# Kernel tuning notes

Measured on AMD Instinct MI355X. Metric: run time of the kernel, lower is better.

Reference implementation:

```python
import jax, jax.numpy as jnp
import numpy as np

N_NODES = 100000
HIDDEN = 64
N_LAYERS = 4
N_EDGES = 800000
EPS = 1e-5  # equinox RMSNorm default


def rmsnorm(x, w):
    # per-node RMSNorm over last dim, learned scale, no bias
    inv = jax.lax.rsqrt(jnp.mean(x * x, axis=-1, keepdims=True) + EPS)
    return x * inv * w


def setup_inputs() -> dict:
    key = jax.random.key(0)
    ks = jax.random.split(key, 5)
    x = jax.random.normal(ks[0], (N_NODES, HIDDEN), dtype=jnp.float32)
    # eqx Linear weight (out,in), init ~ U(-1/sqrt(in), 1/sqrt(in)); randn*scale is fine for a baseline
    scale = 1.0 / np.sqrt(HIDDEN)
    conv_w = jax.random.normal(ks[1], (N_LAYERS, HIDDEN, HIDDEN), dtype=jnp.float32) * scale
    hid_w = jax.random.normal(ks[2], (N_LAYERS, HIDDEN, HIDDEN), dtype=jnp.float32) * scale
    conv_norm_w = jnp.ones((N_LAYERS, HIDDEN), dtype=jnp.float32)
    hid_norm_w = jnp.ones((N_LAYERS, HIDDEN), dtype=jnp.float32)
    row = jax.random.randint(ks[3], (N_EDGES,), 0, N_NODES, dtype=jnp.int32)
    col = jax.random.randint(ks[4], (N_EDGES,), 0, N_NODES, dtype=jnp.int32)
    return {"x": x, "conv_w": conv_w, "conv_norm_w": conv_norm_w,
            "hid_w": hid_w, "hid_norm_w": hid_norm_w, "row": row, "col": col}


def reference(x, conv_w, conv_norm_w, hid_w, hid_norm_w, row, col):
    n_nodes = x.shape[0]

    def step(h, params):
        cw, cnw, hw, hnw = params
        # GConvLayer: linear (no bias) -> relu -> sparse adjacency aggregation -> residual RMSNorm
        m = jax.nn.relu(h @ cw.T)                                  # [n_nodes, d]
        agg = jax.ops.segment_sum(m[col], row, num_segments=n_nodes)  # a @ m (unweighted COO)
        h = rmsnorm(h + agg, cnw)
        # HiddenLayer: linear -> relu -> residual RMSNorm
        y = jax.nn.relu(h @ hw.T)
        h = rmsnorm(h + y, hnw)
        return h, None

    x, _ = jax.lax.scan(step, x, (conv_w, conv_norm_w, hid_w, hid_norm_w))
    return x
```

## Files before the change

### kernel.cpp

```cpp
#include <hip/hip_runtime.h>
#include <hip/hip_bf16.h>

#define HIDDEN 64
#define EPS 1e-5f
#define NPB 64
#define WST 72

typedef __attribute__((ext_vector_type(8))) short bf16x8;
typedef __attribute__((ext_vector_type(4))) float f32x4;

__device__ __forceinline__ unsigned short f2b(float x) {
    __hip_bfloat16 b = __float2bfloat16(x);
    return *(unsigned short*)&b;
}
__device__ __forceinline__ float b2f(unsigned short u) {
    unsigned int ui = (unsigned int)u << 16;
    return *(float*)&ui;
}
__device__ __forceinline__ float b2f_lo(unsigned int u) { unsigned int ui = u << 16; return *(float*)&ui; }
__device__ __forceinline__ float b2f_hi(unsigned int u) { unsigned int ui = u & 0xffff0000u; return *(float*)&ui; }


__global__ __launch_bounds__(256) void hist_rank_kernel(const int* __restrict__ row,
                                                        int* __restrict__ cnt,
                                                        int* __restrict__ erank, int e) {
    int stride = gridDim.x * blockDim.x;
    for (int i = blockIdx.x * blockDim.x + threadIdx.x; i < e; i += stride) {
        int r = row[i];
        erank[i] = atomicAdd(&cnt[r], 1);
    }
}

__global__ __launch_bounds__(256) void block_sum_kernel(const int* __restrict__ cnt,
                                                        int* __restrict__ bsum, int n) {
    __shared__ int wsum[4];
    int tid = threadIdx.x;
    int i = blockIdx.x * 256 + tid;
    int v = (i < n) ? cnt[i] : 0;
#pragma unroll
    for (int off = 32; off > 0; off >>= 1) v += __shfl_xor(v, off, 64);
    if ((tid & 63) == 0) wsum[tid >> 6] = v;
    __syncthreads();
    if (tid == 0) bsum[blockIdx.x] = wsum[0] + wsum[1] + wsum[2] + wsum[3];
}

__global__ __launch_bounds__(256) void scan_final_kernel(const int* __restrict__ cnt,
                                                         const int* __restrict__ bsum,
                                                         int* __restrict__ row_ptr,
                                                         int n, int nb) {
    __shared__ int wred[4];
    __shared__ int wsum[4];
    __shared__ int wexcl[4];
    __shared__ int s_prev;
    __shared__ int s_tot;
    int b = blockIdx.x;
    int tid = threadIdx.x;
    int lane = tid & 63;
    int w = tid >> 6;
    int acc = 0;
    for (int j = tid; j < b; j += 256) acc += bsum[j];
#pragma unroll
    for (int off = 32; off > 0; off >>= 1) acc += __shfl_xor(acc, off, 64);
    if (lane == 0) wred[w] = acc;
    int i = b * 256 + tid;
    int v = (i < n) ? cnt[i] : 0;
    int sc = v;
#pragma unroll
    for (int off = 1; off < 64; off <<= 1) {
        int t = __shfl_up(sc, off, 64);
        if (lane >= off) sc += t;
    }
    if (lane == 63) wsum[w] = sc;
    __syncthreads();
    if (tid == 0) {
        s_prev = wred[0] + wred[1] + wred[2] + wred[3];
        int a = 0;
#pragma unroll
        for (int j = 0; j < 4; j++) { wexcl[j] = a; a += wsum[j]; }
        s_tot = a;
    }
    __syncthreads();
    if (i < n) row_ptr[i] = s_prev + wexcl[w] + (sc - v);
    if (b == nb - 1 && tid == 0) row_ptr[n] = s_prev + s_tot;
}

__global__ __launch_bounds__(256) void fill_kernel(const int* __restrict__ row,
                                                   const int* __restrict__ col,
                                                   const int* __restrict__ row_ptr,
                                                   const int* __restrict__ erank,
                                                   int* __restrict__ ecol, int e, int n) {
    int cls = blockIdx.x & 7;
    int sub = blockIdx.x >> 3;
    int nsub = gridDim.x >> 3;
    int lo = (int)(((long long)n * cls) >> 3);
    int hi = (int)(((long long)n * (cls + 1)) >> 3);
    for (int i = sub * 256 + threadIdx.x; i < e; i += nsub * 256) {
        int r = row[i];
        if (r >= lo && r < hi) {
            int pos = row_ptr[r] + erank[i];
            ecol[pos] = col[i];
        }
    }
}

__global__ __launch_bounds__(256) void wconv_kernel(const float* __restrict__ cw,
                                                    const float* __restrict__ hw,
                                                    unsigned short* __restrict__ wbt, int L) {
    int idx = blockIdx.x * blockDim.x + threadIdx.x;
    int total = 2 * L * 4096;
    if (idx >= total) return;
    int mat = idx >> 12;
    int rem = idx & 4095;
    const float* src = (mat < L) ? (cw + (size_t)mat * 4096) : (hw + (size_t)(mat - L) * 4096);
    wbt[idx] = f2b(src[rem]);
}


__device__ __forceinline__ void mfma_tile(const unsigned short* s_a,
                                          const unsigned short* s_b,
                                          int l16, int quad, int wbase, f32x4 acc[4]) {
    const unsigned short* ap = &s_a[(size_t)(wbase + l16) * WST + quad * 8];
    const unsigned short* bp = &s_b[(size_t)l16 * WST + quad * 8];
#pragma unroll
    for (int kt = 0; kt < 2; kt++) {
        bf16x8 a = *(const bf16x8*)(ap + kt * 32);
#pragma unroll
        for (int nt = 0; nt < 4; nt++) {
            bf16x8 b = *(const bf16x8*)(bp + (size_t)nt * 16 * WST + kt * 32);
            acc[nt] = __builtin_amdgcn_mfma_f32_16x16x32_bf16(a, b, acc[nt], 0, 0, 0);
        }
    }
}

__device__ __forceinline__ void stage_wb(const unsigned short* __restrict__ wsrc,
                                         unsigned short* s_wb, int tid) {
    for (int i = tid; i < 512; i += 256) {
        int r = i >> 3, seg = i & 7;
        *(uint4*)(&s_wb[r * WST + seg * 8]) = ((const uint4*)(wsrc + r * 64))[seg];
    }
}


__global__ __launch_bounds__(256) void mm_relu_kernel(const float* __restrict__ h,
                                                      const unsigned short* __restrict__ wb,
                                                      __hip_bfloat16* __restrict__ m, int n) {
    __shared__ unsigned short s_hb[NPB * WST];
    __shared__ unsigned short s_wb[64 * WST];
    int tid = threadIdx.x;
    int base = blockIdx.x * NPB;
    stage_wb(wb, s_wb, tid);
    for (int i = tid; i < 512; i += 256) {
        int r = i >> 3, seg = i & 7;
        if (base + r < n) {
            const float4* hp = (const float4*)(h + (size_t)(base + r) * HIDDEN + seg * 8);
            float4 ha = hp[0], hb = hp[1];
            uint4 p;
            p.x = (unsigned int)f2b(ha.x) | ((unsigned int)f2b(ha.y) << 16);
            p.y = (unsigned int)f2b(ha.z) | ((unsigned int)f2b(ha.w) << 16);
            p.z = (unsigned int)f2b(hb.x) | ((unsigned int)f2b(hb.y) << 16);
            p.w = (unsigned int)f2b(hb.z) | ((unsigned int)f2b(hb.w) << 16);
            *(uint4*)(&s_hb[r * WST + seg * 8]) = p;
        } else {
            *(uint4*)(&s_hb[r * WST + seg * 8]) = make_uint4(0u, 0u, 0u, 0u);
        }
    }
    __syncthreads();
    int lane = tid & 63, wave = tid >> 6;
    int quad = lane >> 4, l16 = lane & 15;
    int wbase = wave * 16;
    f32x4 acc[4];
    acc[0] = (f32x4){0.f,0.f,0.f,0.f}; acc[1] = (f32x4){0.f,0.f,0.f,0.f};
    acc[2] = (f32x4){0.f,0.f,0.f,0.f}; acc[3] = (f32x4){0.f,0.f,0.f,0.f};
    mfma_tile(s_hb, s_wb, l16, quad, wbase, acc);
    unsigned short* mo = (unsigned short*)m;
#pragma unroll
    for (int r = 0; r < 4; r++) {
        int node = base + wbase + quad * 4 + r;
        if (node < n) {
#pragma unroll
            for (int nt = 0; nt < 4; nt++)
                mo[(size_t)node * HIDDEN + nt * 16 + l16] = f2b(fmaxf(acc[nt][r], 0.f));
        }
    }
}


__global__ __launch_bounds__(256) void fused_layer_kernel(
        const float* hf, const __hip_bfloat16* hb_in,
        const __hip_bfloat16* __restrict__ m_in,
        const unsigned short* __restrict__ hwb,
        const unsigned short* cwb_next,
        const int* __restrict__ row_ptr, const int* __restrict__ ecol,
        const float* __restrict__ cnw, const float* __restrict__ hnw,
        float* out_f32, __hip_bfloat16* hb_new, __hip_bfloat16* m_out, int n) {
    __shared__ unsigned short s_hb[NPB * WST];
    __shared__ unsigned short s_wb[64 * WST];
    __shared__ unsigned short s_wb2[64 * WST];
    int tid = threadIdx.x;
    int base = blockIdx.x * NPB;
    int lane = tid & 63, wave = tid >> 6;

    stage_wb(hwb, s_wb, tid);
    if (cwb_next) stage_wb(cwb_next, s_wb2, tid);

    int grp = lane >> 3;
    int sl = lane & 7;
    int sbase = grp * 8;
    const float4* cp = (const float4*)(cnw + 8 * sl);
    float4 c0 = cp[0], c1 = cp[1];
    const unsigned short* mi = (const unsigned short*)m_in;

#pragma unroll
    for (int rnd = 0; rnd < 2; rnd++) {
        int nl = wave * 16 + rnd * 8 + grp;
        int node = base + nl;
        uint4 pb = make_uint4(0u, 0u, 0u, 0u);
        if (node < n) {
            float s[8];
            if (hf) {
                const float4* hp = (const float4*)(hf + (size_t)node * HIDDEN + 8 * sl);
                float4 v0 = hp[0], v1 = hp[1];
                s[0] = v0.x; s[1] = v0.y; s[2] = v0.z; s[3] = v0.w;
                s[4] = v1.x; s[5] = v1.y; s[6] = v1.z; s[7] = v1.w;
            } else {
                uint4 u = *(const uint4*)((const unsigned short*)hb_in + (size_t)node * HIDDEN + 8 * sl);
                s[0] = b2f_lo(u.x); s[1] = b2f_hi(u.x);
                s[2] = b2f_lo(u.y); s[3] = b2f_hi(u.y);
                s[4] = b2f_lo(u.z); s[5] = b2f_hi(u.z);
                s[6] = b2f_lo(u.w); s[7] = b2f_hi(u.w);
            }
            int beg = row_ptr[node];
            int end = row_ptr[node + 1];
            float p0[8], p1[8];
#pragma unroll
            for (int q = 0; q < 8; q++) { p0[q] = 0.f; p1[q] = 0.f; }
            for (int b0 = beg; b0 < end; b0 += 8) {
                int idx = b0 + sl;
                int myc = ecol[idx < end ? idx : end - 1];
                int cnt = end - b0;
                if (cnt > 8) cnt = 8;
                int c[8];
#pragma unroll
                for (int j = 0; j < 8; j++) c[j] = __shfl(myc, sbase + j, 64);
                uint4 u[8];
#pragma unroll
                for (int j = 0; j < 8; j++)
                    u[j] = *(const uint4*)(mi + (size_t)c[j] * HIDDEN + 8 * sl);
#pragma unroll
                for (int j = 0; j < 8; j++) {
                    bool ok = j < cnt;
                    float* p = (j & 1) ? p1 : p0;
                    p[0] += ok ? b2f_lo(u[j].x) : 0.f;
                    p[1] += ok ? b2f_hi(u[j].x) : 0.f;
                    p[2] += ok ? b2f_lo(u[j].y) : 0.f;
                    p[3] += ok ? b2f_hi(u[j].y) : 0.f;
                    p[4] += ok ? b2f_lo(u[j].z) : 0.f;
                    p[5] += ok ? b2f_hi(u[j].z) : 0.f;
                    p[6] += ok ? b2f_lo(u[j].w) : 0.f;
                    p[7] += ok ? b2f_hi(u[j].w) : 0.f;
                }
            }
            float ss = 0.f;
#pragma unroll
            for (int q = 0; q < 8; q++) {
                s[q] += p0[q] + p1[q];
                ss += s[q] * s[q];
            }
#pragma unroll
            for (int off = 4; off > 0; off >>= 1) ss += __shfl_xor(ss, off, 64);
            float inv = rsqrtf(ss * (1.0f / 64.0f) + EPS);
            pb.x = (unsigned int)f2b(s[0] * inv * c0.x) | ((unsigned int)f2b(s[1] * inv * c0.y) << 16);
            pb.y = (unsigned int)f2b(s[2] * inv * c0.z) | ((unsigned int)f2b(s[3] * inv * c0.w) << 16);
            pb.z = (unsigned int)f2b(s[4] * inv * c1.x) | ((unsigned int)f2b(s[5] * inv * c1.y) << 16);
            pb.w = (unsigned int)f2b(s[6] * inv * c1.z) | ((unsigned int)f2b(s[7] * inv * c1.w) << 16);
        }
        *(uint4*)(&s_hb[(size_t)nl * WST + 8 * sl]) = pb;
    }
    __syncthreads();

    int quad = lane >> 4, l16 = lane & 15;
    int wbase = wave * 16;
    f32x4 acc[4];
    acc[0] = (f32x4){0.f,0.f,0.f,0.f}; acc[1] = (f32x4){0.f,0.f,0.f,0.f};
    acc[2] = (f32x4){0.f,0.f,0.f,0.f}; acc[3] = (f32x4){0.f,0.f,0.f,0.f};
    mfma_tile(s_hb, s_wb, l16, quad, wbase, acc);

    float hv[4][4];
    float ssq[4] = {0.f, 0.f, 0.f, 0.f};
#pragma unroll
    for (int r = 0; r < 4; r++) {
        int nl = wbase + quad * 4 + r;
#pragma unroll
        for (int nt = 0; nt < 4; nt++) {
            float hres = b2f(s_hb[(size_t)nl * WST + nt * 16 + l16]);
            float v = hres + fmaxf(acc[nt][r], 0.f);
            hv[r][nt] = v;
            ssq[r] += v * v;
        }
    }
#pragma unroll
    for (int mk = 1; mk <= 8; mk <<= 1) {
#pragma unroll
        for (int r = 0; r < 4; r++) ssq[r] += __shfl_xor(ssq[r], mk, 64);
    }
    float nwv[4];
#pragma unroll
    for (int nt = 0; nt < 4; nt++) nwv[nt] = hnw[nt * 16 + l16];
#pragma unroll
    for (int r = 0; r < 4; r++) {
        float inv = rsqrtf(ssq[r] * (1.0f / 64.0f) + EPS);
#pragma unroll
        for (int nt = 0; nt < 4; nt++) hv[r][nt] *= inv * nwv[nt];
    }
    if (out_f32) {
#pragma unroll
        for (int r = 0; r < 4; r++) {
            int node = base + wbase + quad * 4 + r;
            if (node < n) {
#pragma unroll
                for (int nt = 0; nt < 4; nt++)
                    out_f32[(size_t)node * HIDDEN + nt * 16 + l16] = hv[r][nt];
            }
        }
    }
    if (hb_new) {
        unsigned short* ho = (unsigned short*)hb_new;
#pragma unroll
        for (int r = 0; r < 4; r++) {
            int node = base + wbase + quad * 4 + r;
            if (node < n) {
#pragma unroll
                for (int nt = 0; nt < 4; nt++)
                    ho[(size_t)node * HIDDEN + nt * 16 + l16] = f2b(hv[r][nt]);
            }
        }
    }

    if (!m_out) return;

#pragma unroll
    for (int r = 0; r < 4; r++) {
        int nl = wbase + quad * 4 + r;
#pragma unroll
        for (int nt = 0; nt < 4; nt++)
            s_hb[(size_t)nl * WST + nt * 16 + l16] = f2b(hv[r][nt]);
    }

    f32x4 acc2[4];
    acc2[0] = (f32x4){0.f,0.f,0.f,0.f}; acc2[1] = (f32x4){0.f,0.f,0.f,0.f};
    acc2[2] = (f32x4){0.f,0.f,0.f,0.f}; acc2[3] = (f32x4){0.f,0.f,0.f,0.f};
    mfma_tile(s_hb, s_wb2, l16, quad, wbase, acc2);
    unsigned short* mo = (unsigned short*)m_out;
#pragma unroll
    for (int r = 0; r < 4; r++) {
        int node = base + wbase + quad * 4 + r;
        if (node < n) {
#pragma unroll
            for (int nt = 0; nt < 4; nt++)
                mo[(size_t)node * HIDDEN + nt * 16 + l16] = f2b(fmaxf(acc2[nt][r], 0.f));
        }
    }
}


static inline size_t align_up(size_t x, size_t a) { return (x + a - 1) & ~(a - 1); }

extern "C" void kernel_launch(void* const* d_in, const int* in_sizes, int n_in,
                              void* d_out, int out_size, void* d_ws, size_t ws_size,
                              hipStream_t stream) {
    const float* x       = (const float*)d_in[0];
    const float* conv_w  = (const float*)d_in[1];
    const float* conv_nw = (const float*)d_in[2];
    const float* hid_w   = (const float*)d_in[3];
    const float* hid_nw  = (const float*)d_in[4];
    const int*   row     = (const int*)d_in[5];
    const int*   col     = (const int*)d_in[6];
    float* out = (float*)d_out;

    const int n = in_sizes[0] / HIDDEN;
    const int e = in_sizes[5];
    const int L = in_sizes[1] / 4096;

    size_t off = 0;
    char* ws = (char*)d_ws;
    __hip_bfloat16* mA = (__hip_bfloat16*)(ws + off);  off = align_up(off + (size_t)n * HIDDEN * 2, 16);
    __hip_bfloat16* mB = (__hip_bfloat16*)(ws + off);  off = align_up(off + (size_t)n * HIDDEN * 2, 16);
    __hip_bfloat16* hb1 = (__hip_bfloat16*)(ws + off); off = align_up(off + (size_t)n * HIDDEN * 2, 16);
    __hip_bfloat16* hb2 = (__hip_bfloat16*)(ws + off); off = align_up(off + (size_t)n * HIDDEN * 2, 16);
    unsigned short* wbt = (unsigned short*)(ws + off); off = align_up(off + (size_t)2 * L * 4096 * 2, 16);
    int* row_ptr = (int*)(ws + off);           off = align_up(off + (size_t)(n + 1) * 4, 16);
    int* cnt = (int*)(ws + off);               off = align_up(off + (size_t)n * 4, 16);
    int* bsum = (int*)(ws + off);              off = align_up(off + (size_t)1024 * 4, 16);
    int* erank = (int*)(ws + off);             off = align_up(off + (size_t)e * 4, 16);
    int* ecol = (int*)(ws + off);              off = align_up(off + (size_t)e * 4, 16);

    const int nb = (n + 255) / 256;

    hipMemsetAsync(cnt, 0, (size_t)n * 4, stream);
    hist_rank_kernel<<<1024, 256, 0, stream>>>(row, cnt, erank, e);
    block_sum_kernel<<<nb, 256, 0, stream>>>(cnt, bsum, n);
    scan_final_kernel<<<nb, 256, 0, stream>>>(cnt, bsum, row_ptr, n, nb);
    fill_kernel<<<1024, 256, 0, stream>>>(row, col, row_ptr, erank, ecol, e, n);

    wconv_kernel<<<(2 * L * 4096 + 255) / 256, 256, 0, stream>>>(conv_w, hid_w, wbt, L);

    const int blocks = (n + NPB - 1) / NPB;

    mm_relu_kernel<<<blocks, 256, 0, stream>>>(x, wbt, mA, n);

    const __hip_bfloat16* mi = mA;
    __hip_bfloat16* mo = mB;
    __hip_bfloat16* hin = nullptr;
    __hip_bfloat16* hout = hb1;
    for (int l = 0; l < L; l++) {
        bool last = (l == L - 1);
        fused_layer_kernel<<<blocks, 256, 0, stream>>>(
            (l == 0) ? x : nullptr, hin, mi,
            wbt + (size_t)(L + l) * 4096,
            last ? nullptr : (wbt + (size_t)(l + 1) * 4096),
            row_ptr, ecol,
            conv_nw + (size_t)l * HIDDEN, hid_nw + (size_t)l * HIDDEN,
            last ? out : nullptr,
            last ? nullptr : hout,
            last ? nullptr : mo, n);
        __hip_bfloat16* tmp = (__hip_bfloat16*)mi; mi = mo; mo = tmp;
        hin = hout;
        hout = (hout == hb1) ? hb2 : hb1;
    }
}
```

Before: 275.1 us.

## Use 4 lanes per node in gather with prefetched edge indices; load next-layer weights to registers

The gather/aggregation phase now assigns 4 lanes per node, each handling 16 features with two 16-byte loads per neighbor. This replaces the old 8 lanes per node over two rounds. The next batch of edge column indices is prefetched to overlap index loads with the gathers. The second shared-memory weight buffer is removed: the next layer's conv weights are loaded from global memory straight into MFMA B-fragment registers. This cuts LDS usage, which may raise occupancy, at the cost of more registers per thread and fewer loads in flight per batch of edges.

```diff
diff --git a/kernel.cpp b/kernel.cpp
--- a/kernel.cpp
+++ b/kernel.cpp
@@ -19,6 +19,9 @@
 }
 __device__ __forceinline__ float b2f_lo(unsigned int u) { unsigned int ui = u << 16; return *(float*)&ui; }
 __device__ __forceinline__ float b2f_hi(unsigned int u) { unsigned int ui = u & 0xffff0000u; return *(float*)&ui; }
+__device__ __forceinline__ unsigned int pk2(float a, float b) {
+    return (unsigned int)f2b(a) | ((unsigned int)f2b(b) << 16);
+}
 
 
 __global__ __launch_bounds__(256) void hist_rank_kernel(const int* __restrict__ row,
@@ -140,6 +143,17 @@
     }
 }
 
+__device__ __forceinline__ void acc8(float* p, uint4 u, bool ok) {
+    p[0] += ok ? b2f_lo(u.x) : 0.f;
+    p[1] += ok ? b2f_hi(u.x) : 0.f;
+    p[2] += ok ? b2f_lo(u.y) : 0.f;
+    p[3] += ok ? b2f_hi(u.y) : 0.f;
+    p[4] += ok ? b2f_lo(u.z) : 0.f;
+    p[5] += ok ? b2f_hi(u.z) : 0.f;
+    p[6] += ok ? b2f_lo(u.w) : 0.f;
+    p[7] += ok ? b2f_hi(u.w) : 0.f;
+}
+
 
 __global__ __launch_bounds__(256) void mm_relu_kernel(const float* __restrict__ h,
                                                       const unsigned short* __restrict__ wb,
@@ -155,10 +169,10 @@
             const float4* hp = (const float4*)(h + (size_t)(base + r) * HIDDEN + seg * 8);
             float4 ha = hp[0], hb = hp[1];
             uint4 p;
-            p.x = (unsigned int)f2b(ha.x) | ((unsigned int)f2b(ha.y) << 16);
-            p.y = (unsigned int)f2b(ha.z) | ((unsigned int)f2b(ha.w) << 16);
-            p.z = (unsigned int)f2b(hb.x) | ((unsigned int)f2b(hb.y) << 16);
-            p.w = (unsigned int)f2b(hb.z) | ((unsigned int)f2b(hb.w) << 16);
+            p.x = pk2(ha.x, ha.y);
+            p.y = pk2(ha.z, ha.w);
+            p.z = pk2(hb.x, hb.y);
+            p.w = pk2(hb.z, hb.w);
             *(uint4*)(&s_hb[r * WST + seg * 8]) = p;
         } else {
             *(uint4*)(&s_hb[r * WST + seg * 8]) = make_uint4(0u, 0u, 0u, 0u);
@@ -195,87 +209,96 @@
         float* out_f32, __hip_bfloat16* hb_new, __hip_bfloat16* m_out, int n) {
     __shared__ unsigned short s_hb[NPB * WST];
     __shared__ unsigned short s_wb[64 * WST];
-    __shared__ unsigned short s_wb2[64 * WST];
     int tid = threadIdx.x;
     int base = blockIdx.x * NPB;
     int lane = tid & 63, wave = tid >> 6;
 
     stage_wb(hwb, s_wb, tid);
-    if (cwb_next) stage_wb(cwb_next, s_wb2, tid);
-
-    int grp = lane >> 3;
-    int sl = lane & 7;
-    int sbase = grp * 8;
-    const float4* cp = (const float4*)(cnw + 8 * sl);
-    float4 c0 = cp[0], c1 = cp[1];
+
+    int g = lane >> 2;
+    int sl = lane & 3;
+    int gb = lane & ~3;
+    int nl = wave * 16 + g;
+    int node = base + nl;
+
+    const float4* cp = (const float4*)(cnw + 16 * sl);
+    float4 c0 = cp[0], c1 = cp[1], c2 = cp[2], c3 = cp[3];
     const unsigned short* mi = (const unsigned short*)m_in;
 
-#pragma unroll
-    for (int rnd = 0; rnd < 2; rnd++) {
-        int nl = wave * 16 + rnd * 8 + grp;
-        int node = base + nl;
-        uint4 pb = make_uint4(0u, 0u, 0u, 0u);
-        if (node < n) {
-            float s[8];
-            if (hf) {
-                const float4* hp = (const float4*)(hf + (size_t)node * HIDDEN + 8 * sl);
-                float4 v0 = hp[0], v1 = hp[1];
-                s[0] = v0.x; s[1] = v0.y; s[2] = v0.z; s[3] = v0.w;
-                s[4] = v1.x; s[5] = v1.y; s[6] = v1.z; s[7] = v1.w;
-            } else {
-                uint4 u = *(const uint4*)((const unsigned short*)hb_in + (size_t)node * HIDDEN + 8 * sl);
-                s[0] = b2f_lo(u.x); s[1] = b2f_hi(u.x);
-                s[2] = b2f_lo(u.y); s[3] = b2f_hi(u.y);
-                s[4] = b2f_lo(u.z); s[5] = b2f_hi(u.z);
-                s[6] = b2f_lo(u.w); s[7] = b2f_hi(u.w);
+    uint4 q0 = make_uint4(0u, 0u, 0u, 0u);
+    uint4 q1 = make_uint4(0u, 0u, 0u, 0u);
+    if (node < n) {
+        float p[16];
+        if (hf) {
+            const float4* hp = (const float4*)(hf + (size_t)node * HIDDEN + 16 * sl);
+            float4 v0 = hp[0], v1 = hp[1], v2 = hp[2], v3 = hp[3];
+            p[0]=v0.x;  p[1]=v0.y;  p[2]=v0.z;  p[3]=v0.w;
+            p[4]=v1.x;  p[5]=v1.y;  p[6]=v1.z;  p[7]=v1.w;
+            p[8]=v2.x;  p[9]=v2.y;  p[10]=v2.z; p[11]=v2.w;
+            p[12]=v3.x; p[13]=v3.y; p[14]=v3.z; p[15]=v3.w;
+        } else {
+            const uint4* hp = (const uint4*)((const unsigned short*)hb_in + (size_t)node * HIDDEN + 16 * sl);
+            uint4 u0 = hp[0], u1 = hp[1];
+            p[0]=b2f_lo(u0.x);  p[1]=b2f_hi(u0.x);
+            p[2]=b2f_lo(u0.y);  p[3]=b2f_hi(u0.y);
+            p[4]=b2f_lo(u0.z);  p[5]=b2f_hi(u0.z);
+            p[6]=b2f_lo(u0.w);  p[7]=b2f_hi(u0.w);
+            p[8]=b2f_lo(u1.x);  p[9]=b2f_hi(u1.x);
+            p[10]=b2f_lo(u1.y); p[11]=b2f_hi(u1.y);
+            p[12]=b2f_lo(u1.z); p[13]=b2f_hi(u1.z);
+            p[14]=b2f_lo(u1.w); p[15]=b2f_hi(u1.w);
+        }
+        int beg = row_ptr[node];
+        int end = row_ptr[node + 1];
+        int myc = 0;
+        if (beg < end) {
+            int idx = beg + sl;
+            myc = ecol[idx < end ? idx : end - 1];
+        }
+        for (int b0 = beg; b0 < end; b0 += 4) {
+            int nxt = b0 + 4;
+            int nmyc = 0;
+            if (nxt < end) {
+                int idx = nxt + sl;
+                nmyc = ecol[idx < end ? idx : end - 1];
             }
-            int beg = row_ptr[node];
-            int end = row_ptr[node + 1];
-            float p0[8], p1[8];
-#pragma unroll
-            for (int q = 0; q < 8; q++) { p0[q] = 0.f; p1[q] = 0.f; }
-            for (int b0 = beg; b0 < end; b0 += 8) {
-                int idx = b0 + sl;
-                int myc = ecol[idx < end ? idx : end - 1];
-                int cnt = end - b0;
-                if (cnt > 8) cnt = 8;
-                int c[8];
-#pragma unroll
-                for (int j = 0; j < 8; j++) c[j] = __shfl(myc, sbase + j, 64);
-                uint4 u[8];
-#pragma unroll
-                for (int j = 0; j < 8; j++)
-                    u[j] = *(const uint4*)(mi + (size_t)c[j] * HIDDEN + 8 * sl);
-#pragma unroll
-                for (int j = 0; j < 8; j++) {
-                    bool ok = j < cnt;
-                    float* p = (j & 1) ? p1 : p0;
-                    p[0] += ok ? b2f_lo(u[j].x) : 0.f;
-                    p[1] += ok ? b2f_hi(u[j].x) : 0.f;
-                    p[2] += ok ? b2f_lo(u[j].y) : 0.f;
-                    p[3] += ok ? b2f_hi(u[j].y) : 0.f;
-                    p[4] += ok ? b2f_lo(u[j].z) : 0.f;
-                    p[5] += ok ? b2f_hi(u[j].z) : 0.f;
-                    p[6] += ok ? b2f_lo(u[j].w) : 0.f;
-                    p[7] += ok ? b2f_hi(u[j].w) : 0.f;
-                }
+            int cnt = end - b0;
+            if (cnt > 4) cnt = 4;
+            int cj[4];
+#pragma unroll
+            for (int j = 0; j < 4; j++) cj[j] = __shfl(myc, gb + j, 64);
+            uint4 ua[4], ub[4];
+#pragma unroll
+            for (int j = 0; j < 4; j++) {
+                const uint4* mp = (const uint4*)(mi + (size_t)cj[j] * HIDDEN + 16 * sl);
+                ua[j] = mp[0];
+                ub[j] = mp[1];
             }
-            float ss = 0.f;
-#pragma unroll
-            for (int q = 0; q < 8; q++) {
-                s[q] += p0[q] + p1[q];
-                ss += s[q] * s[q];
+#pragma unroll
+            for (int j = 0; j < 4; j++) {
+                bool ok = j < cnt;
+                acc8(p, ua[j], ok);
+                acc8(p + 8, ub[j], ok);
             }
-#pragma unroll
-            for (int off = 4; off > 0; off >>= 1) ss += __shfl_xor(ss, off, 64);
-            float inv = rsqrtf(ss * (1.0f / 64.0f) + EPS);
-            pb.x = (unsigned int)f2b(s[0] * inv * c0.x) | ((unsigned int)f2b(s[1] * inv * c0.y) << 16);
-            pb.y = (unsigned int)f2b(s[2] * inv * c0.z) | ((unsigned int)f2b(s[3] * inv * c0.w) << 16);
-            pb.z = (unsigned int)f2b(s[4] * inv * c1.x) | ((unsigned int)f2b(s[5] * inv * c1.y) << 16);
-            pb.w = (unsigned int)f2b(s[6] * inv * c1.z) | ((unsigned int)f2b(s[7] * inv * c1.w) << 16);
-        }
-        *(uint4*)(&s_hb[(size_t)nl * WST + 8 * sl]) = pb;
-    }
+            myc = nmyc;
+        }
+        float ss = 0.f;
+#pragma unroll
+        for (int k = 0; k < 16; k++) ss += p[k] * p[k];
+        ss += __shfl_xor(ss, 1, 64);
+        ss += __shfl_xor(ss, 2, 64);
+        float inv = rsqrtf(ss * (1.0f / 64.0f) + EPS);
+        q0.x = pk2(p[0]*inv*c0.x,  p[1]*inv*c0.y);
+        q0.y = pk2(p[2]*inv*c0.z,  p[3]*inv*c0.w);
+        q0.z = pk2(p[4]*inv*c1.x,  p[5]*inv*c1.y);
+        q0.w = pk2(p[6]*inv*c1.z,  p[7]*inv*c1.w);
+        q1.x = pk2(p[8]*inv*c2.x,  p[9]*inv*c2.y);
+        q1.y = pk2(p[10]*inv*c2.z, p[11]*inv*c2.w);
+        q1.z = pk2(p[12]*inv*c3.x, p[13]*inv*c3.y);
+        q1.w = pk2(p[14]*inv*c3.z, p[15]*inv*c3.w);
+    }
+    *(uint4*)(&s_hb[(size_t)nl * WST + 16 * sl]) = q0;
+    *(uint4*)(&s_hb[(size_t)nl * WST + 16 * sl + 8]) = q1;
     __syncthreads();
 
     int quad = lane >> 4, l16 = lane & 15;
@@ -289,10 +312,10 @@
     float ssq[4] = {0.f, 0.f, 0.f, 0.f};
 #pragma unroll
     for (int r = 0; r < 4; r++) {
-        int nl = wbase + quad * 4 + r;
+        int nr = wbase + quad * 4 + r;
 #pragma unroll
         for (int nt = 0; nt < 4; nt++) {
-            float hres = b2f(s_hb[(size_t)nl * WST + nt * 16 + l16]);
+            float hres = b2f(s_hb[(size_t)nr * WST + nt * 16 + l16]);
             float v = hres + fmaxf(acc[nt][r], 0.f);
             hv[r][nt] = v;
             ssq[r] += v * v;
@@ -315,11 +338,11 @@
     if (out_f32) {
 #pragma unroll
         for (int r = 0; r < 4; r++) {
-            int node = base + wbase + quad * 4 + r;
-            if (node < n) {
+            int nd = base + wbase + quad * 4 + r;
+            if (nd < n) {
 #pragma unroll
                 for (int nt = 0; nt < 4; nt++)
-                    out_f32[(size_t)node * HIDDEN + nt * 16 + l16] = hv[r][nt];
+                    out_f32[(size_t)nd * HIDDEN + nt * 16 + l16] = hv[r][nt];
             }
         }
     }
@@ -327,37 +350,57 @@
         unsigned short* ho = (unsigned short*)hb_new;
 #pragma unroll
         for (int r = 0; r < 4; r++) {
-            int node = base + wbase + quad * 4 + r;
-            if (node < n) {
+            int nd = base + wbase + quad * 4 + r;
+            if (nd < n) {
 #pragma unroll
                 for (int nt = 0; nt < 4; nt++)
-                    ho[(size_t)node * HIDDEN + nt * 16 + l16] = f2b(hv[r][nt]);
+                    ho[(size_t)nd * HIDDEN + nt * 16 + l16] = f2b(hv[r][nt]);
             }
         }
     }
 
     if (!m_out) return;
 
+    bf16x8 wf[8];
+    {
+        const unsigned short* wp = cwb_next + (size_t)l16 * 64 + quad * 8;
+#pragma unroll
+        for (int nt = 0; nt < 4; nt++) {
+#pragma unroll
+            for (int kt = 0; kt < 2; kt++)
+                wf[nt * 2 + kt] = *(const bf16x8*)(wp + (size_t)nt * 16 * 64 + kt * 32);
+        }
+    }
+
 #pragma unroll
     for (int r = 0; r < 4; r++) {
-        int nl = wbase + quad * 4 + r;
+        int nr = wbase + quad * 4 + r;
 #pragma unroll
         for (int nt = 0; nt < 4; nt++)
-            s_hb[(size_t)nl * WST + nt * 16 + l16] = f2b(hv[r][nt]);
+            s_hb[(size_t)nr * WST + nt * 16 + l16] = f2b(hv[r][nt]);
     }
 
     f32x4 acc2[4];
     acc2[0] = (f32x4){0.f,0.f,0.f,0.f}; acc2[1] = (f32x4){0.f,0.f,0.f,0.f};
     acc2[2] = (f32x4){0.f,0.f,0.f,0.f}; acc2[3] = (f32x4){0.f,0.f,0.f,0.f};
-    mfma_tile(s_hb, s_wb2, l16, quad, wbase, acc2);
+    {
+        const unsigned short* ap = &s_hb[(size_t)(wbase + l16) * WST + quad * 8];
+#pragma unroll
+        for (int kt = 0; kt < 2; kt++) {
+            bf16x8 a = *(const bf16x8*)(ap + kt * 32);
+#pragma unroll
+            for (int nt = 0; nt < 4; nt++)
+                acc2[nt] = __builtin_amdgcn_mfma_f32_16x16x32_bf16(a, wf[nt * 2 + kt], acc2[nt], 0, 0, 0);
+        }
+    }
     unsigned short* mo = (unsigned short*)m_out;
 #pragma unroll
     for (int r = 0; r < 4; r++) {
-        int node = base + wbase + quad * 4 + r;
-        if (node < n) {
+        int nd = base + wbase + quad * 4 + r;
+        if (nd < n) {
 #pragma unroll
             for (int nt = 0; nt < 4; nt++)
-                mo[(size_t)node * HIDDEN + nt * 16 + l16] = f2b(fmaxf(acc2[nt][r], 0.f));
+                mo[(size_t)nd * HIDDEN + nt * 16 + l16] = f2b(fmaxf(acc2[nt][r], 0.f));
         }
     }
 }
```

Result: slower. 291.0 us (+5.8%).
